# Kernel optimization log

Hardware: AMD Instinct MI355X
Metric: run time of the kernel (lower is better)

## Reference

```python
import jax, jax.numpy as jnp
import numpy as np

EPS = 1e-5
B, H, W = 256, 64, 64
HASH_NUM, SPLIT_NUM, IN_CH = 48, 16, 3


def conv(x, w, b):
    y = jax.lax.conv_general_dilated(x, w, (1, 1), 'VALID',
                                     dimension_numbers=('NCHW', 'OIHW', 'NCHW'))
    return y + b[None, :, None, None]


def bn2d(x, g, b):
    m = x.mean((0, 2, 3), keepdims=True)
    v = x.var((0, 2, 3), keepdims=True)
    return (x - m) * jax.lax.rsqrt(v + EPS) * g[None, :, None, None] + b[None, :, None, None]


def bn1d(x, g, b):
    m = x.mean(0)
    v = x.var(0)
    return (x - m) * jax.lax.rsqrt(v + EPS) * g + b


def maxpool2(x):
    return jax.lax.reduce_window(x, -jnp.inf, jax.lax.max,
                                 (1, 1, 2, 2), (1, 1, 2, 2), 'VALID')


def setup_inputs() -> dict:
    key = jax.random.key(0)
    ks = jax.random.split(key, 16)
    s = 0.1
    inp = {
        'x': jax.random.normal(ks[0], (B, IN_CH, H, W), jnp.float32),
        'conv1_w': jax.random.normal(ks[1], (20, IN_CH, 3, 3), jnp.float32) * s,
        'conv1_b': jnp.zeros((20,), jnp.float32),
        'bn1_g': jnp.ones((20,), jnp.float32),
        'bn1_b': jnp.zeros((20,), jnp.float32),
        'conv2_w': jax.random.normal(ks[2], (40, 20, 2, 2), jnp.float32) * s,
        'conv2_b': jnp.zeros((40,), jnp.float32),
        'bn2_g': jnp.ones((40,), jnp.float32),
        'bn2_b': jnp.zeros((40,), jnp.float32),
        'conv3_w': jax.random.normal(ks[3], (60, 40, 2, 2), jnp.float32) * s,
        'conv3_b': jnp.zeros((60,), jnp.float32),
        'bn3_g': jnp.ones((60,), jnp.float32),
        'bn3_b': jnp.zeros((60,), jnp.float32),
        # LocallyConnected2d: weight [1, 80, 60, 6, 6, 4], bias [1, 80, 6, 6]
        'lc_w': jax.random.normal(ks[4], (1, 80, 60, 6, 6, 4), jnp.float32) * s,
        'lc_b': jax.random.normal(ks[5], (1, 80, 6, 6), jnp.float32) * s,
        'bn4_g': jnp.ones((80,), jnp.float32),
        'bn4_b': jnp.zeros((80,), jnp.float32),
        # Linear(5820 -> 768): torch stores weight as [out, in]
        'fc_w': jax.random.normal(ks[6], (HASH_NUM * SPLIT_NUM, 5820), jnp.float32) * 0.01,
        'fc_b': jnp.zeros((HASH_NUM * SPLIT_NUM,), jnp.float32),
        'bn5_g': jnp.ones((HASH_NUM * SPLIT_NUM,), jnp.float32),
        'bn5_b': jnp.zeros((HASH_NUM * SPLIT_NUM,), jnp.float32),
        # per-hash fuse linears Linear(split_num, 1), stacked -> [48, 16], [48]
        'fuse_w': jax.random.normal(ks[7], (HASH_NUM, SPLIT_NUM), jnp.float32) * s,
        'fuse_b': jnp.zeros((HASH_NUM,), jnp.float32),
    }
    return inp


def reference(x, conv1_w, conv1_b, bn1_g, bn1_b,
              conv2_w, conv2_b, bn2_g, bn2_b,
              conv3_w, conv3_b, bn3_g, bn3_b,
              lc_w, lc_b, bn4_g, bn4_b,
              fc_w, fc_b, bn5_g, bn5_b,
              fuse_w, fuse_b):
    h = maxpool2(jax.nn.relu(bn2d(conv(x, conv1_w, conv1_b), bn1_g, bn1_b)))   # [B,20,31,31]
    h = maxpool2(jax.nn.relu(bn2d(conv(h, conv2_w, conv2_b), bn2_g, bn2_b)))   # [B,40,15,15]
    h = maxpool2(jax.nn.relu(bn2d(conv(h, conv3_w, conv3_b), bn3_g, bn3_b)))   # [B,60,7,7]
    x1 = h.reshape(h.shape[0], -1)                                             # [B,2940]
    # LocallyConnected2d k=2, s=1: patches [B,60,6,6,4], flatten order (kh,kw)
    p = jnp.stack([h[:, :, 0:6, 0:6], h[:, :, 0:6, 1:7],
                   h[:, :, 1:7, 0:6], h[:, :, 1:7, 1:7]], axis=-1)
    lc = jnp.einsum('bcijk,ocijk->boij', p, lc_w[0]) + lc_b                    # [B,80,6,6]
    lc = jax.nn.relu(bn2d(lc, bn4_g, bn4_b))
    x2 = lc.reshape(lc.shape[0], -1)                                           # [B,2880]
    feat = jnp.concatenate([x1, x2], axis=1)                                   # [B,5820]
    y = feat @ fc_w.T + fc_b                                                   # [B,768]
    y = jax.nn.relu(bn1d(y, bn5_g, bn5_b))
    yr = y.reshape(y.shape[0], HASH_NUM, SPLIT_NUM)                            # [B,48,16]
    out = jnp.einsum('bhs,hs->bh', yr, fuse_w) + fuse_b                        # [B,48]
    return out
```

## Files before the change

kernel.cpp:

```cpp
#include <hip/hip_runtime.h>

#define EPSF 1e-5f

#define P1S 0
#define P1Q 81920
#define P2S 163840
#define P2Q 204800
#define P3S 245760
#define P3Q 261120
#define P4S 276480
#define P4Q 279360
#define SC1 282240
#define SH1 282260
#define SC2 282280
#define SH2 282320
#define SC3 282360
#define SH3 282420
#define SC4 282480
#define SH4 282560
#define SC5 282640
#define SH5 283408

#define OFF_A 524288
#define OFF_B 20205568
#define OFF_C 25125888
#define OFF_D 25878528
#define OFF_Y 26615808

#define KP 6144

__device__ __forceinline__ void blockReduce2(float& v1, float& v2) {
  __syncthreads();
  #pragma unroll
  for (int off = 32; off > 0; off >>= 1) {
    v1 += __shfl_down(v1, off);
    v2 += __shfl_down(v2, off);
  }
  __shared__ float s1[4], s2[4];
  const int wid = threadIdx.x >> 6, lane = threadIdx.x & 63;
  if (lane == 0) { s1[wid] = v1; s2[wid] = v2; }
  __syncthreads();
  if (threadIdx.x == 0) { v1 = s1[0]+s1[1]+s1[2]+s1[3]; v2 = s2[0]+s2[1]+s2[2]+s2[3]; }
}

__device__ __forceinline__ unsigned short f2bf(float f) {
  unsigned int u = __float_as_uint(f);
  return (unsigned short)((u + 0x7FFFu + ((u >> 16) & 1u)) >> 16);
}

__global__ __launch_bounds__(256) void conv1_stats_kernel(
    const float* __restrict__ x, const float* __restrict__ w, const float* __restrict__ cb,
    float* __restrict__ ps, float* __restrict__ pq) {
  const int sp = blockIdx.x * 256 + threadIdx.x;
  const int c0 = blockIdx.y * 5, b = blockIdx.z;
  __shared__ float wsh[5][27];
  if (threadIdx.x < 135) wsh[threadIdx.x / 27][threadIdx.x % 27] = w[c0 * 27 + threadIdx.x];
  __syncthreads();
  float acc[5] = {};
  if (sp < 3844) {
    const int oy = sp / 62, ox = sp - oy * 62;
    const float* xb = x + (size_t)b * 3 * 4096 + oy * 64 + ox;
    #pragma unroll
    for (int ic = 0; ic < 3; ic++)
      #pragma unroll
      for (int ky = 0; ky < 3; ky++)
        #pragma unroll
        for (int kx = 0; kx < 3; kx++) {
          const float v = xb[ic * 4096 + ky * 64 + kx];
          const int tap = (ic * 3 + ky) * 3 + kx;
          #pragma unroll
          for (int ol = 0; ol < 5; ol++)
            acc[ol] = fmaf(v, wsh[ol][tap], acc[ol]);
        }
    #pragma unroll
    for (int ol = 0; ol < 5; ol++) acc[ol] += cb[c0 + ol];
  }
  #pragma unroll
  for (int ol = 0; ol < 5; ol++) {
    float v1 = acc[ol], v2 = acc[ol] * acc[ol];
    blockReduce2(v1, v2);
    if (threadIdx.x == 0) {
      ps[(c0 + ol) * 4096 + b * 16 + blockIdx.x] = v1;
      pq[(c0 + ol) * 4096 + b * 16 + blockIdx.x] = v2;
    }
  }
}

__global__ __launch_bounds__(256) void convpool1_kernel(
    const float* __restrict__ x, const float* __restrict__ w, const float* __restrict__ cb,
    const float* __restrict__ scale, const float* __restrict__ shift,
    float* __restrict__ out) {
  const int sp = blockIdx.x * 256 + threadIdx.x;
  const int c0 = blockIdx.y * 5, b = blockIdx.z;
  __shared__ float wsh[5][27];
  if (threadIdx.x < 135) wsh[threadIdx.x / 27][threadIdx.x % 27] = w[c0 * 27 + threadIdx.x];
  __syncthreads();
  if (sp >= 961) return;
  const int py = sp / 31, px = sp - py * 31;
  const float* xb = x + (size_t)b * 3 * 4096 + (2 * py) * 64 + 2 * px;
  float acc[5][4] = {};
  #pragma unroll
  for (int ic = 0; ic < 3; ic++) {
    float v[4][4];
    #pragma unroll
    for (int r = 0; r < 4; r++)
      #pragma unroll
      for (int cc = 0; cc < 4; cc++)
        v[r][cc] = xb[ic * 4096 + r * 64 + cc];
    #pragma unroll
    for (int ol = 0; ol < 5; ol++)
      #pragma unroll
      for (int dy = 0; dy < 2; dy++)
        #pragma unroll
        for (int dx = 0; dx < 2; dx++) {
          float a = acc[ol][dy * 2 + dx];
          #pragma unroll
          for (int ky = 0; ky < 3; ky++)
            #pragma unroll
            for (int kx = 0; kx < 3; kx++)
              a = fmaf(v[dy + ky][dx + kx], wsh[ol][(ic * 3 + ky) * 3 + kx], a);
          acc[ol][dy * 2 + dx] = a;
        }
  }
  #pragma unroll
  for (int ol = 0; ol < 5; ol++) {
    const float sc = scale[c0 + ol];
    const float sh = fmaf(cb[c0 + ol], sc, shift[c0 + ol]);
    float m = -1e30f;
    #pragma unroll
    for (int q = 0; q < 4; q++)
      m = fmaxf(m, fmaxf(fmaf(acc[ol][q], sc, sh), 0.f));
    out[(size_t)(b * 20 + c0 + ol) * 961 + sp] = m;
  }
}

__global__ __launch_bounds__(256) void conv2_kernel(
    const float* __restrict__ in, const float* __restrict__ w, const float* __restrict__ cb,
    float* __restrict__ out, float* __restrict__ ps, float* __restrict__ pq) {
  const int sp = blockIdx.x * 256 + threadIdx.x;
  const int c0 = blockIdx.y * 8, b = blockIdx.z;
  __shared__ float4 wsh4[8][20];
  for (int e = threadIdx.x; e < 160; e += 256)
    wsh4[e / 20][e % 20] = ((const float4*)w)[c0 * 20 + e];
  __syncthreads();
  float acc[8] = {};
  if (sp < 900) {
    const int oy = sp / 30, ox = sp - oy * 30;
    const float* ib = in + (size_t)b * 20 * 961 + oy * 31 + ox;
    #pragma unroll 4
    for (int ic = 0; ic < 20; ic++) {
      const float v0 = ib[ic * 961];
      const float v1 = ib[ic * 961 + 1];
      const float v2 = ib[ic * 961 + 31];
      const float v3 = ib[ic * 961 + 32];
      #pragma unroll
      for (int ol = 0; ol < 8; ol++) {
        const float4 wv = wsh4[ol][ic];
        acc[ol] = fmaf(v0, wv.x, acc[ol]);
        acc[ol] = fmaf(v1, wv.y, acc[ol]);
        acc[ol] = fmaf(v2, wv.z, acc[ol]);
        acc[ol] = fmaf(v3, wv.w, acc[ol]);
      }
    }
    #pragma unroll
    for (int ol = 0; ol < 8; ol++) {
      acc[ol] += cb[c0 + ol];
      out[(size_t)(b * 40 + c0 + ol) * 900 + sp] = acc[ol];
    }
  }
  #pragma unroll
  for (int ol = 0; ol < 8; ol++) {
    float v1 = acc[ol], v2 = acc[ol] * acc[ol];
    blockReduce2(v1, v2);
    if (threadIdx.x == 0) {
      ps[(c0 + ol) * 1024 + b * 4 + blockIdx.x] = v1;
      pq[(c0 + ol) * 1024 + b * 4 + blockIdx.x] = v2;
    }
  }
}

__global__ __launch_bounds__(256) void conv3_kernel(
    const float* __restrict__ in, const float* __restrict__ w, const float* __restrict__ cb,
    float* __restrict__ out, float* __restrict__ ps, float* __restrict__ pq) {
  const int sp = threadIdx.x;
  const int c0 = blockIdx.y * 6, b = blockIdx.z;
  __shared__ float4 wsh4[6][40];
  if (threadIdx.x < 240)
    wsh4[threadIdx.x / 40][threadIdx.x % 40] = ((const float4*)w)[c0 * 40 + threadIdx.x];
  __syncthreads();
  float acc[6] = {};
  if (sp < 196) {
    const int oy = sp / 14, ox = sp - oy * 14;
    const float* ib = in + (size_t)b * 40 * 225 + oy * 15 + ox;
    #pragma unroll 4
    for (int ic = 0; ic < 40; ic++) {
      const float v0 = ib[ic * 225];
      const float v1 = ib[ic * 225 + 1];
      const float v2 = ib[ic * 225 + 15];
      const float v3 = ib[ic * 225 + 16];
      #pragma unroll
      for (int ol = 0; ol < 6; ol++) {
        const float4 wv = wsh4[ol][ic];
        acc[ol] = fmaf(v0, wv.x, acc[ol]);
        acc[ol] = fmaf(v1, wv.y, acc[ol]);
        acc[ol] = fmaf(v2, wv.z, acc[ol]);
        acc[ol] = fmaf(v3, wv.w, acc[ol]);
      }
    }
    #pragma unroll
    for (int ol = 0; ol < 6; ol++) {
      acc[ol] += cb[c0 + ol];
      out[(size_t)(b * 60 + c0 + ol) * 196 + sp] = acc[ol];
    }
  }
  #pragma unroll
  for (int ol = 0; ol < 6; ol++) {
    float v1 = acc[ol], v2 = acc[ol] * acc[ol];
    blockReduce2(v1, v2);
    if (threadIdx.x == 0) {
      ps[(c0 + ol) * 256 + b] = v1;
      pq[(c0 + ol) * 256 + b] = v2;
    }
  }
}

template<int SLOTS>
__global__ __launch_bounds__(256) void bnfin_kernel(
    const float* __restrict__ ps, const float* __restrict__ pq,
    const float* __restrict__ g, const float* __restrict__ bet,
    float* __restrict__ scale, float* __restrict__ shift, float invN) {
  const int c = blockIdx.x;
  float s = 0.f, q = 0.f;
  for (int i = threadIdx.x; i < SLOTS; i += 256) { s += ps[c * SLOTS + i]; q += pq[c * SLOTS + i]; }
  blockReduce2(s, q);
  if (threadIdx.x == 0) {
    const float m = s * invN;
    const float var = q * invN - m * m;
    const float sc = g[c] * rsqrtf(var + EPSF);
    scale[c] = sc;
    shift[c] = bet[c] - m * sc;
  }
}

template<int C, int Hin, int Win, int Hout, int Wout>
__global__ __launch_bounds__(256) void bnrelupool_kernel(
    const float* __restrict__ in, float* __restrict__ out,
    const float* __restrict__ scale, const float* __restrict__ shift, int total) {
  const int idx = blockIdx.x * 256 + threadIdx.x;
  if (idx >= total) return;
  const int px = idx % Wout;
  int t = idx / Wout;
  const int py = t % Hout; t /= Hout;
  const int c = t % C;
  const int b = t / C;
  const float sc = scale[c], sh = shift[c];
  const float* p = in + ((size_t)(b * C + c) * Hin + 2 * py) * Win + 2 * px;
  const float2 r0 = *(const float2*)p;
  const float2 r1 = *(const float2*)(p + Win);
  float a0 = fmaxf(fmaf(r0.x, sc, sh), 0.f);
  float a1 = fmaxf(fmaf(r0.y, sc, sh), 0.f);
  float a2 = fmaxf(fmaf(r1.x, sc, sh), 0.f);
  float a3 = fmaxf(fmaf(r1.y, sc, sh), 0.f);
  out[idx] = fmaxf(fmaxf(a0, a1), fmaxf(a2, a3));
}

__global__ __launch_bounds__(256) void transpose_h_kernel(
    const float* __restrict__ in, float* __restrict__ out) {
  __shared__ float tile[64][65];
  const int lx = threadIdx.x & 63, ly = threadIdx.x >> 6;
  const int c0 = blockIdx.x * 64;
  const int r0 = blockIdx.y * 64;
  #pragma unroll
  for (int i = 0; i < 16; i++) {
    const int b = r0 + ly + i * 4;
    const int cp = c0 + lx;
    tile[ly + i * 4][lx] = (cp < 2940) ? in[(size_t)b * 2940 + cp] : 0.f;
  }
  __syncthreads();
  #pragma unroll
  for (int i = 0; i < 16; i++) {
    const int cp = c0 + ly + i * 4;
    if (cp < 2940) out[(size_t)cp * 256 + r0 + lx] = tile[lx][ly + i * 4];
  }
}

__global__ __launch_bounds__(256) void lc2_kernel(
    const float* __restrict__ hT, const float* __restrict__ w, const float* __restrict__ lb,
    float* __restrict__ outT, float* __restrict__ ps, float* __restrict__ pq) {
  const int sp = blockIdx.x;
  const int o0 = blockIdx.y * 8;
  const int b = threadIdx.x;
  __shared__ float wsh[8 * 240];
  for (int e = threadIdx.x; e < 1920; e += 256) {
    const int ol = e / 240, ck = e - ol * 240;
    const int c = ck >> 2, k = ck & 3;
    wsh[e] = w[((size_t)((o0 + ol) * 60 + c) * 36 + sp) * 4 + k];
  }
  __syncthreads();
  const int i = sp / 6, j = sp - i * 6;
  const int pos0 = i * 7 + j;
  float acc[8] = {};
  #pragma unroll 4
  for (int c = 0; c < 60; c++) {
    const float h0 = hT[(size_t)(c * 49 + pos0) * 256 + b];
    const float h1 = hT[(size_t)(c * 49 + pos0 + 1) * 256 + b];
    const float h2 = hT[(size_t)(c * 49 + pos0 + 7) * 256 + b];
    const float h3 = hT[(size_t)(c * 49 + pos0 + 8) * 256 + b];
    #pragma unroll
    for (int ol = 0; ol < 8; ol++) {
      const float* wp = &wsh[ol * 240 + c * 4];
      acc[ol] = fmaf(h0, wp[0], acc[ol]);
      acc[ol] = fmaf(h1, wp[1], acc[ol]);
      acc[ol] = fmaf(h2, wp[2], acc[ol]);
      acc[ol] = fmaf(h3, wp[3], acc[ol]);
    }
  }
  #pragma unroll
  for (int ol = 0; ol < 8; ol++) {
    const int o = o0 + ol;
    const float val = acc[ol] + lb[o * 36 + sp];
    outT[(size_t)(o * 36 + sp) * 256 + b] = val;
    float v1 = val, v2 = val * val;
    blockReduce2(v1, v2);
    if (threadIdx.x == 0) { ps[o * 36 + sp] = v1; pq[o * 36 + sp] = v2; }
  }
}

__global__ __launch_bounds__(256) void lcpost2_kernel(
    const float* __restrict__ inT, float* __restrict__ out,
    const float* __restrict__ scale, const float* __restrict__ shift) {
  __shared__ float tile[64][65];
  const int lx = threadIdx.x & 63, ly = threadIdx.x >> 6;
  const int k0 = blockIdx.x * 64;
  const int b0 = blockIdx.y * 64;
  #pragma unroll
  for (int i = 0; i < 16; i++) {
    const int k = k0 + ly + i * 4;
    const int o = k / 36;
    const float v = inT[(size_t)k * 256 + b0 + lx];
    tile[ly + i * 4][lx] = fmaxf(fmaf(v, scale[o], shift[o]), 0.f);
  }
  __syncthreads();
  #pragma unroll
  for (int i = 0; i < 16; i++) {
    const int b = b0 + ly + i * 4;
    out[(size_t)b * 2880 + k0 + lx] = tile[lx][ly + i * 4];
  }
}

__global__ __launch_bounds__(256) void pack_feat_kernel(
    const float* __restrict__ h, const float* __restrict__ x2, unsigned short* __restrict__ fB) {
  const int idx = blockIdx.x * 256 + threadIdx.x;
  const int b = idx / 1536, kq = idx - b * 1536;
  const int k0 = kq * 4;
  ushort4 o;
  float v[4];
  #pragma unroll
  for (int q = 0; q < 4; q++) {
    const int k = k0 + q;
    v[q] = (k < 2940) ? h[(size_t)b * 2940 + k]
         : (k < 5820) ? x2[(size_t)b * 2880 + (k - 2940)] : 0.f;
  }
  o.x = f2bf(v[0]); o.y = f2bf(v[1]); o.z = f2bf(v[2]); o.w = f2bf(v[3]);
  *(ushort4*)&fB[(size_t)b * KP + k0] = o;
}

__global__ __launch_bounds__(256) void pack_w_kernel(
    const float* __restrict__ W, unsigned short* __restrict__ WBp) {
  const int idx = blockIdx.x * 256 + threadIdx.x;
  const int n = idx / 1536, kq = idx - n * 1536;
  const int k0 = kq * 4;
  ushort4 o;
  float v[4];
  #pragma unroll
  for (int q = 0; q < 4; q++) {
    const int k = k0 + q;
    v[q] = (k < 5820) ? W[(size_t)n * 5820 + k] : 0.f;
  }
  o.x = f2bf(v[0]); o.y = f2bf(v[1]); o.z = f2bf(v[2]); o.w = f2bf(v[3]);
  *(ushort4*)&WBp[(size_t)n * KP + k0] = o;
}

typedef __attribute__((ext_vector_type(4))) float f32x4;
typedef __attribute__((ext_vector_type(8))) short bf16x8;

__global__ __launch_bounds__(256) void fc_mfma_kernel(
    const unsigned short* __restrict__ fB, const unsigned short* __restrict__ WBp,
    float* __restrict__ Y) {
  const int wid = threadIdx.x >> 6, l = threadIdx.x & 63;
  const int wy = wid >> 1, wx = wid & 1;
  const int m0 = blockIdx.x * 64 + wy * 32;
  const int n0 = blockIdx.y * 64 + wx * 32;
  const int lrow = l & 15, lk = (l >> 4) * 8;
  const unsigned short* ap = fB + (size_t)(m0 + lrow) * KP + lk;
  const unsigned short* bp = WBp + (size_t)(n0 + lrow) * KP + lk;
  f32x4 acc[2][2] = {};
  const int kbase = blockIdx.z * 1536;
  #pragma unroll 4
  for (int s = 0; s < 48; s++) {
    const int k = kbase + s * 32;
    const bf16x8 a0 = *(const bf16x8*)(ap + k);
    const bf16x8 a1 = *(const bf16x8*)(ap + 16 * KP + k);
    const bf16x8 b0 = *(const bf16x8*)(bp + k);
    const bf16x8 b1 = *(const bf16x8*)(bp + 16 * KP + k);
    acc[0][0] = __builtin_amdgcn_mfma_f32_16x16x32_bf16(a0, b0, acc[0][0], 0, 0, 0);
    acc[0][1] = __builtin_amdgcn_mfma_f32_16x16x32_bf16(a0, b1, acc[0][1], 0, 0, 0);
    acc[1][0] = __builtin_amdgcn_mfma_f32_16x16x32_bf16(a1, b0, acc[1][0], 0, 0, 0);
    acc[1][1] = __builtin_amdgcn_mfma_f32_16x16x32_bf16(a1, b1, acc[1][1], 0, 0, 0);
  }
  const int orow = (l >> 4) * 4, ocol = l & 15;
  #pragma unroll
  for (int fi = 0; fi < 2; fi++)
    #pragma unroll
    for (int fj = 0; fj < 2; fj++)
      #pragma unroll
      for (int r = 0; r < 4; r++)
        atomicAdd(&Y[(size_t)(m0 + fi * 16 + orow + r) * 768 + n0 + fj * 16 + ocol],
                  acc[fi][fj][r]);
}

__global__ __launch_bounds__(256) void bn5_stats_kernel(
    const float* __restrict__ Y, const float* __restrict__ g, const float* __restrict__ bet,
    float* __restrict__ scale, float* __restrict__ shift) {
  const int tx = threadIdx.x & 63, ty = threadIdx.x >> 6;
  const int n = blockIdx.x * 64 + tx;
  float s = 0.f, q = 0.f;
  for (int bi = 0; bi < 64; bi++) {
    const float v = Y[(size_t)(bi * 4 + ty) * 768 + n];
    s += v; q += v * v;
  }
  __shared__ float rs[4][64], rq[4][64];
  rs[ty][tx] = s; rq[ty][tx] = q;
  __syncthreads();
  if (ty == 0) {
    s = rs[0][tx] + rs[1][tx] + rs[2][tx] + rs[3][tx];
    q = rq[0][tx] + rq[1][tx] + rq[2][tx] + rq[3][tx];
    const float m = s * (1.f / 256.f);
    const float var = q * (1.f / 256.f) - m * m;
    const float sc = g[n] * rsqrtf(var + EPSF);
    scale[n] = sc;
    shift[n] = bet[n] - m * sc;
  }
}

__global__ __launch_bounds__(256) void final_kernel(
    const float* __restrict__ Y, const float* __restrict__ scale, const float* __restrict__ shift,
    const float* __restrict__ fw, const float* __restrict__ fb, float* __restrict__ out) {
  const int idx = blockIdx.x * 256 + threadIdx.x;
  const int b = idx / 48, hh = idx - b * 48;
  const float* yb = Y + (size_t)b * 768 + hh * 16;
  const float* sc = scale + hh * 16;
  const float* sh = shift + hh * 16;
  const float* w = fw + hh * 16;
  float acc = fb[hh];
  #pragma unroll
  for (int s = 0; s < 16; s++)
    acc += fmaxf(fmaf(yb[s], sc[s], sh[s]), 0.f) * w[s];
  out[idx] = acc;
}

extern "C" void kernel_launch(void* const* d_in, const int* in_sizes, int n_in,
                              void* d_out, int out_size, void* d_ws, size_t ws_size,
                              hipStream_t stream) {
  const float* x   = (const float*)d_in[0];
  const float* c1w = (const float*)d_in[1];
  const float* c1b = (const float*)d_in[2];
  const float* g1  = (const float*)d_in[3];
  const float* b1  = (const float*)d_in[4];
  const float* c2w = (const float*)d_in[5];
  const float* c2b = (const float*)d_in[6];
  const float* g2  = (const float*)d_in[7];
  const float* b2  = (const float*)d_in[8];
  const float* c3w = (const float*)d_in[9];
  const float* c3b = (const float*)d_in[10];
  const float* g3  = (const float*)d_in[11];
  const float* b3  = (const float*)d_in[12];
  const float* lcw = (const float*)d_in[13];
  const float* lcb = (const float*)d_in[14];
  const float* g4  = (const float*)d_in[15];
  const float* b4  = (const float*)d_in[16];
  const float* fcw = (const float*)d_in[17];
  const float* g5  = (const float*)d_in[19];
  const float* b5  = (const float*)d_in[20];
  const float* fw  = (const float*)d_in[21];
  const float* fb  = (const float*)d_in[22];

  float* ws = (float*)d_ws;
  float* A  = ws + OFF_A;
  float* B_ = ws + OFF_B;
  float* C_ = ws + OFF_C;
  float* D_ = ws + OFF_D;
  float* Y  = ws + OFF_Y;
  unsigned short* featB = (unsigned short*)A;
  unsigned short* WB    = (unsigned short*)(A + 786432);

  hipMemsetAsync(Y, 0, 196608 * sizeof(float), stream);

  conv1_stats_kernel<<<dim3(16, 4, 256), 256, 0, stream>>>(x, c1w, c1b, ws + P1S, ws + P1Q);
  bnfin_kernel<4096><<<20, 256, 0, stream>>>(ws + P1S, ws + P1Q, g1, b1, ws + SC1, ws + SH1, 1.f / 984064.f);
  convpool1_kernel<<<dim3(4, 4, 256), 256, 0, stream>>>(x, c1w, c1b, ws + SC1, ws + SH1, B_);
  conv2_kernel<<<dim3(4, 5, 256), 256, 0, stream>>>(B_, c2w, c2b, A, ws + P2S, ws + P2Q);
  bnfin_kernel<1024><<<40, 256, 0, stream>>>(ws + P2S, ws + P2Q, g2, b2, ws + SC2, ws + SH2, 1.f / 230400.f);
  bnrelupool_kernel<40, 30, 30, 15, 15><<<9000, 256, 0, stream>>>(A, B_, ws + SC2, ws + SH2, 2304000);
  conv3_kernel<<<dim3(1, 10, 256), 256, 0, stream>>>(B_, c3w, c3b, A, ws + P3S, ws + P3Q);
  bnfin_kernel<256><<<60, 256, 0, stream>>>(ws + P3S, ws + P3Q, g3, b3, ws + SC3, ws + SH3, 1.f / 50176.f);
  bnrelupool_kernel<60, 14, 14, 7, 7><<<2940, 256, 0, stream>>>(A, C_, ws + SC3, ws + SH3, 752640);
  transpose_h_kernel<<<dim3(46, 4), 256, 0, stream>>>(C_, B_);
  lc2_kernel<<<dim3(36, 10), 256, 0, stream>>>(B_, lcw, lcb, A, ws + P4S, ws + P4Q);
  bnfin_kernel<36><<<80, 256, 0, stream>>>(ws + P4S, ws + P4Q, g4, b4, ws + SC4, ws + SH4, 1.f / 9216.f);
  lcpost2_kernel<<<dim3(45, 4), 256, 0, stream>>>(A, D_, ws + SC4, ws + SH4);
  pack_feat_kernel<<<1536, 256, 0, stream>>>(C_, D_, featB);
  pack_w_kernel<<<4608, 256, 0, stream>>>(fcw, WB);
  fc_mfma_kernel<<<dim3(4, 12, 4), 256, 0, stream>>>(featB, WB, Y);
  bn5_stats_kernel<<<12, 256, 0, stream>>>(Y, g5, b5, ws + SC5, ws + SH5);
  final_kernel<<<48, 256, 0, stream>>>(Y, ws + SC5, ws + SH5, fw, fb, (float*)d_out);
}
```

Measured before the change: 412.5 us.

## Fuse conv2 with BN-ReLU-pool by recomputing conv, and tile conv1 stats per pool window

The conv2 stage becomes two passes: a stats kernel that only reduces sums, then a convpool kernel that recomputes the convolution and applies BN, ReLU and 2x2 max-pool in registers. This removes the full-resolution conv2 output write, its reread and the separate bnrelupool launch. The conv1 stats kernel now has each thread compute a 2x2 output block from a shared 4x4 input window, and both stats kernels use per-wave shuffle reductions instead of block reductions. The cost is doing the conv2 arithmetic twice and holding more accumulators per thread.

```diff
diff --git a/kernel.cpp b/kernel.cpp
--- a/kernel.cpp
+++ b/kernel.cpp
@@ -43,6 +43,14 @@
   if (threadIdx.x == 0) { v1 = s1[0]+s1[1]+s1[2]+s1[3]; v2 = s2[0]+s2[1]+s2[2]+s2[3]; }
 }
 
+__device__ __forceinline__ void waveReduce2(float& a, float& b) {
+  #pragma unroll
+  for (int off = 32; off > 0; off >>= 1) {
+    a += __shfl_down(a, off);
+    b += __shfl_down(b, off);
+  }
+}
+
 __device__ __forceinline__ unsigned short f2bf(float f) {
   unsigned int u = __float_as_uint(f);
   return (unsigned short)((u + 0x7FFFu + ((u >> 16) & 1u)) >> 16);
@@ -56,32 +64,53 @@
   __shared__ float wsh[5][27];
   if (threadIdx.x < 135) wsh[threadIdx.x / 27][threadIdx.x % 27] = w[c0 * 27 + threadIdx.x];
   __syncthreads();
-  float acc[5] = {};
-  if (sp < 3844) {
-    const int oy = sp / 62, ox = sp - oy * 62;
-    const float* xb = x + (size_t)b * 3 * 4096 + oy * 64 + ox;
-    #pragma unroll
-    for (int ic = 0; ic < 3; ic++)
-      #pragma unroll
-      for (int ky = 0; ky < 3; ky++)
+  float s[5] = {}, q[5] = {};
+  if (sp < 961) {
+    const int py = sp / 31, px = sp - py * 31;
+    const float* xb = x + (size_t)b * 3 * 4096 + (2 * py) * 64 + 2 * px;
+    float acc[5][4] = {};
+    #pragma unroll
+    for (int ic = 0; ic < 3; ic++) {
+      float v[4][4];
+      #pragma unroll
+      for (int r = 0; r < 4; r++)
         #pragma unroll
-        for (int kx = 0; kx < 3; kx++) {
-          const float v = xb[ic * 4096 + ky * 64 + kx];
-          const int tap = (ic * 3 + ky) * 3 + kx;
+        for (int cc = 0; cc < 4; cc++)
+          v[r][cc] = xb[ic * 4096 + r * 64 + cc];
+      #pragma unroll
+      for (int ol = 0; ol < 5; ol++)
+        #pragma unroll
+        for (int dy = 0; dy < 2; dy++)
           #pragma unroll
-          for (int ol = 0; ol < 5; ol++)
-            acc[ol] = fmaf(v, wsh[ol][tap], acc[ol]);
-        }
-    #pragma unroll
-    for (int ol = 0; ol < 5; ol++) acc[ol] += cb[c0 + ol];
-  }
-  #pragma unroll
-  for (int ol = 0; ol < 5; ol++) {
-    float v1 = acc[ol], v2 = acc[ol] * acc[ol];
-    blockReduce2(v1, v2);
-    if (threadIdx.x == 0) {
-      ps[(c0 + ol) * 4096 + b * 16 + blockIdx.x] = v1;
-      pq[(c0 + ol) * 4096 + b * 16 + blockIdx.x] = v2;
+          for (int dx = 0; dx < 2; dx++) {
+            float a = acc[ol][dy * 2 + dx];
+            #pragma unroll
+            for (int ky = 0; ky < 3; ky++)
+              #pragma unroll
+              for (int kx = 0; kx < 3; kx++)
+                a = fmaf(v[dy + ky][dx + kx], wsh[ol][(ic * 3 + ky) * 3 + kx], a);
+            acc[ol][dy * 2 + dx] = a;
+          }
+    }
+    #pragma unroll
+    for (int ol = 0; ol < 5; ol++) {
+      const float base = cb[c0 + ol];
+      #pragma unroll
+      for (int k = 0; k < 4; k++) {
+        const float vv = acc[ol][k] + base;
+        s[ol] += vv; q[ol] += vv * vv;
+      }
+    }
+  }
+  #pragma unroll
+  for (int ol = 0; ol < 5; ol++) waveReduce2(s[ol], q[ol]);
+  const int lane = threadIdx.x & 63, wid = threadIdx.x >> 6;
+  if (lane == 0) {
+    const int slot = b * 16 + blockIdx.x * 4 + wid;
+    #pragma unroll
+    for (int ol = 0; ol < 5; ol++) {
+      ps[(c0 + ol) * 4096 + slot] = s[ol];
+      pq[(c0 + ol) * 4096 + slot] = q[ol];
     }
   }
 }
@@ -128,54 +157,120 @@
     const float sh = fmaf(cb[c0 + ol], sc, shift[c0 + ol]);
     float m = -1e30f;
     #pragma unroll
-    for (int q = 0; q < 4; q++)
-      m = fmaxf(m, fmaxf(fmaf(acc[ol][q], sc, sh), 0.f));
+    for (int k = 0; k < 4; k++)
+      m = fmaxf(m, fmaxf(fmaf(acc[ol][k], sc, sh), 0.f));
     out[(size_t)(b * 20 + c0 + ol) * 961 + sp] = m;
   }
 }
 
-__global__ __launch_bounds__(256) void conv2_kernel(
+__global__ __launch_bounds__(256) void conv2_stats_kernel(
     const float* __restrict__ in, const float* __restrict__ w, const float* __restrict__ cb,
-    float* __restrict__ out, float* __restrict__ ps, float* __restrict__ pq) {
-  const int sp = blockIdx.x * 256 + threadIdx.x;
+    float* __restrict__ ps, float* __restrict__ pq) {
+  const int sp = threadIdx.x;
   const int c0 = blockIdx.y * 8, b = blockIdx.z;
   __shared__ float4 wsh4[8][20];
   for (int e = threadIdx.x; e < 160; e += 256)
     wsh4[e / 20][e % 20] = ((const float4*)w)[c0 * 20 + e];
   __syncthreads();
-  float acc[8] = {};
-  if (sp < 900) {
-    const int oy = sp / 30, ox = sp - oy * 30;
-    const float* ib = in + (size_t)b * 20 * 961 + oy * 31 + ox;
+  float s[8] = {}, q[8] = {};
+  if (sp < 225) {
+    const int py = sp / 15, px = sp - py * 15;
+    const float* ib = in + (size_t)b * 20 * 961 + (2 * py) * 31 + 2 * px;
+    float acc[8][4] = {};
     #pragma unroll 4
     for (int ic = 0; ic < 20; ic++) {
-      const float v0 = ib[ic * 961];
-      const float v1 = ib[ic * 961 + 1];
-      const float v2 = ib[ic * 961 + 31];
-      const float v3 = ib[ic * 961 + 32];
+      float v[3][3];
+      #pragma unroll
+      for (int r = 0; r < 3; r++)
+        #pragma unroll
+        for (int cc = 0; cc < 3; cc++)
+          v[r][cc] = ib[ic * 961 + r * 31 + cc];
       #pragma unroll
       for (int ol = 0; ol < 8; ol++) {
         const float4 wv = wsh4[ol][ic];
-        acc[ol] = fmaf(v0, wv.x, acc[ol]);
-        acc[ol] = fmaf(v1, wv.y, acc[ol]);
-        acc[ol] = fmaf(v2, wv.z, acc[ol]);
-        acc[ol] = fmaf(v3, wv.w, acc[ol]);
+        #pragma unroll
+        for (int dy = 0; dy < 2; dy++)
+          #pragma unroll
+          for (int dx = 0; dx < 2; dx++) {
+            float a = acc[ol][dy * 2 + dx];
+            a = fmaf(v[dy][dx],     wv.x, a);
+            a = fmaf(v[dy][dx + 1], wv.y, a);
+            a = fmaf(v[dy + 1][dx], wv.z, a);
+            a = fmaf(v[dy + 1][dx + 1], wv.w, a);
+            acc[ol][dy * 2 + dx] = a;
+          }
       }
     }
     #pragma unroll
     for (int ol = 0; ol < 8; ol++) {
-      acc[ol] += cb[c0 + ol];
-      out[(size_t)(b * 40 + c0 + ol) * 900 + sp] = acc[ol];
+      const float base = cb[c0 + ol];
+      #pragma unroll
+      for (int k = 0; k < 4; k++) {
+        const float vv = acc[ol][k] + base;
+        s[ol] += vv; q[ol] += vv * vv;
+      }
+    }
+  }
+  #pragma unroll
+  for (int ol = 0; ol < 8; ol++) waveReduce2(s[ol], q[ol]);
+  const int lane = threadIdx.x & 63, wid = threadIdx.x >> 6;
+  if (lane == 0) {
+    const int slot = b * 4 + wid;
+    #pragma unroll
+    for (int ol = 0; ol < 8; ol++) {
+      ps[(c0 + ol) * 1024 + slot] = s[ol];
+      pq[(c0 + ol) * 1024 + slot] = q[ol];
+    }
+  }
+}
+
+__global__ __launch_bounds__(256) void convpool2_kernel(
+    const float* __restrict__ in, const float* __restrict__ w, const float* __restrict__ cb,
+    const float* __restrict__ scale, const float* __restrict__ shift,
+    float* __restrict__ out) {
+  const int sp = threadIdx.x;
+  const int c0 = blockIdx.y * 8, b = blockIdx.z;
+  __shared__ float4 wsh4[8][20];
+  for (int e = threadIdx.x; e < 160; e += 256)
+    wsh4[e / 20][e % 20] = ((const float4*)w)[c0 * 20 + e];
+  __syncthreads();
+  if (sp >= 225) return;
+  const int py = sp / 15, px = sp - py * 15;
+  const float* ib = in + (size_t)b * 20 * 961 + (2 * py) * 31 + 2 * px;
+  float acc[8][4] = {};
+  #pragma unroll 4
+  for (int ic = 0; ic < 20; ic++) {
+    float v[3][3];
+    #pragma unroll
+    for (int r = 0; r < 3; r++)
+      #pragma unroll
+      for (int cc = 0; cc < 3; cc++)
+        v[r][cc] = ib[ic * 961 + r * 31 + cc];
+    #pragma unroll
+    for (int ol = 0; ol < 8; ol++) {
+      const float4 wv = wsh4[ol][ic];
+      #pragma unroll
+      for (int dy = 0; dy < 2; dy++)
+        #pragma unroll
+        for (int dx = 0; dx < 2; dx++) {
+          float a = acc[ol][dy * 2 + dx];
+          a = fmaf(v[dy][dx],     wv.x, a);
+          a = fmaf(v[dy][dx + 1], wv.y, a);
+          a = fmaf(v[dy + 1][dx], wv.z, a);
+          a = fmaf(v[dy + 1][dx + 1], wv.w, a);
+          acc[ol][dy * 2 + dx] = a;
+        }
     }
   }
   #pragma unroll
   for (int ol = 0; ol < 8; ol++) {
-    float v1 = acc[ol], v2 = acc[ol] * acc[ol];
-    blockReduce2(v1, v2);
-    if (threadIdx.x == 0) {
-      ps[(c0 + ol) * 1024 + b * 4 + blockIdx.x] = v1;
-      pq[(c0 + ol) * 1024 + b * 4 + blockIdx.x] = v2;
-    }
+    const float sc = scale[c0 + ol];
+    const float sh = fmaf(cb[c0 + ol], sc, shift[c0 + ol]);
+    float m = -1e30f;
+    #pragma unroll
+    for (int k = 0; k < 4; k++)
+      m = fmaxf(m, fmaxf(fmaf(acc[ol][k], sc, sh), 0.f));
+    out[(size_t)(b * 40 + c0 + ol) * 225 + sp] = m;
   }
 }
 
@@ -496,15 +591,15 @@
 
   hipMemsetAsync(Y, 0, 196608 * sizeof(float), stream);
 
-  conv1_stats_kernel<<<dim3(16, 4, 256), 256, 0, stream>>>(x, c1w, c1b, ws + P1S, ws + P1Q);
+  conv1_stats_kernel<<<dim3(4, 4, 256), 256, 0, stream>>>(x, c1w, c1b, ws + P1S, ws + P1Q);
   bnfin_kernel<4096><<<20, 256, 0, stream>>>(ws + P1S, ws + P1Q, g1, b1, ws + SC1, ws + SH1, 1.f / 984064.f);
   convpool1_kernel<<<dim3(4, 4, 256), 256, 0, stream>>>(x, c1w, c1b, ws + SC1, ws + SH1, B_);
-  conv2_kernel<<<dim3(4, 5, 256), 256, 0, stream>>>(B_, c2w, c2b, A, ws + P2S, ws + P2Q);
+  conv2_stats_kernel<<<dim3(1, 5, 256), 256, 0, stream>>>(B_, c2w, c2b, ws + P2S, ws + P2Q);
   bnfin_kernel<1024><<<40, 256, 0, stream>>>(ws + P2S, ws + P2Q, g2, b2, ws + SC2, ws + SH2, 1.f / 230400.f);
-  bnrelupool_kernel<40, 30, 30, 15, 15><<<9000, 256, 0, stream>>>(A, B_, ws + SC2, ws + SH2, 2304000);
-  conv3_kernel<<<dim3(1, 10, 256), 256, 0, stream>>>(B_, c3w, c3b, A, ws + P3S, ws + P3Q);
+  convpool2_kernel<<<dim3(1, 5, 256), 256, 0, stream>>>(B_, c2w, c2b, ws + SC2, ws + SH2, A);
+  conv3_kernel<<<dim3(1, 10, 256), 256, 0, stream>>>(A, c3w, c3b, B_, ws + P3S, ws + P3Q);
   bnfin_kernel<256><<<60, 256, 0, stream>>>(ws + P3S, ws + P3Q, g3, b3, ws + SC3, ws + SH3, 1.f / 50176.f);
-  bnrelupool_kernel<60, 14, 14, 7, 7><<<2940, 256, 0, stream>>>(A, C_, ws + SC3, ws + SH3, 752640);
+  bnrelupool_kernel<60, 14, 14, 7, 7><<<2940, 256, 0, stream>>>(B_, C_, ws + SC3, ws + SH3, 752640);
   transpose_h_kernel<<<dim3(46, 4), 256, 0, stream>>>(C_, B_);
   lc2_kernel<<<dim3(36, 10), 256, 0, stream>>>(B_, lcw, lcb, A, ws + P4S, ws + P4Q);
   bnfin_kernel<36><<<80, 256, 0, stream>>>(ws + P4S, ws + P4Q, g4, b4, ws + SC4, ws + SH4, 1.f / 9216.f);
```

Result: faster. 362.0 us (-12.2%).
